# Optimization experiments

Hardware: AMD Instinct MI355X
Metric: run time of the kernel (lower is better)

## Reference

```python
import jax, jax.numpy as jnp
import numpy as np

TOPK = 13
ALPHA = 1.0
BETA = 6.0
REG_MAX = 16
W_MATCH, W_IOU, W_DFL, W_CONTRAST = 1.0, 7.5, 1.5, 1.0
EPS = 1e-7


def bbox_iou(a, b):
    # a, b: [..., 4] xyxy, broadcastable
    x1 = jnp.maximum(a[..., 0], b[..., 0])
    y1 = jnp.maximum(a[..., 1], b[..., 1])
    x2 = jnp.minimum(a[..., 2], b[..., 2])
    y2 = jnp.minimum(a[..., 3], b[..., 3])
    inter = jnp.clip(x2 - x1, 0.0) * jnp.clip(y2 - y1, 0.0)
    area_a = (a[..., 2] - a[..., 0]) * (a[..., 3] - a[..., 1])
    area_b = (b[..., 2] - b[..., 0]) * (b[..., 3] - b[..., 1])
    return inter / (area_a + area_b - inter + EPS)


def bbox_ciou(a, b):
    iou = bbox_iou(a, b)
    cw = jnp.maximum(a[..., 2], b[..., 2]) - jnp.minimum(a[..., 0], b[..., 0])
    ch = jnp.maximum(a[..., 3], b[..., 3]) - jnp.minimum(a[..., 1], b[..., 1])
    c2 = cw * cw + ch * ch + EPS
    rho2 = ((b[..., 0] + b[..., 2] - a[..., 0] - a[..., 2]) ** 2
            + (b[..., 1] + b[..., 3] - a[..., 1] - a[..., 3]) ** 2) * 0.25
    w1, h1 = a[..., 2] - a[..., 0], a[..., 3] - a[..., 1] + EPS
    w2, h2 = b[..., 2] - b[..., 0], b[..., 3] - b[..., 1] + EPS
    v = (4.0 / (np.pi ** 2)) * (jnp.arctan(w2 / h2) - jnp.arctan(w1 / h1)) ** 2
    alpha = jax.lax.stop_gradient(v / (v - iou + (1.0 + EPS)))
    return iou - rho2 / c2 - v * alpha


def _per_image(scores, boxes, logits, prompt, gts, anchors, stride, img_size):
    # scores [N], boxes [N,4], logits [N,4*REG_MAX], prompt [D], gts [G,4]
    N = scores.shape[0]
    dt = scores.dtype
    inside = ((anchors[None, :, 0] >= gts[:, None, 0]) & (anchors[None, :, 0] <= gts[:, None, 2])
              & (anchors[None, :, 1] >= gts[:, None, 1]) & (anchors[None, :, 1] <= gts[:, None, 3]))  # [G,N]
    ious = bbox_iou(boxes[None, :, :], gts[:, None, :])  # [G,N]
    prob = jax.nn.sigmoid(scores)
    align = jnp.where(inside, jnp.power(prob[None, :], ALPHA) * jnp.power(ious, BETA), -1.0)  # [G,N]
    top_vals, top_idx = jax.lax.top_k(align, TOPK)  # [G,TOPK]
    metric = jax.vmap(lambda i, v: jnp.full((N,), -2.0, dt).at[i].set(v))(top_idx, top_vals)  # [G,N]
    best = metric.max(axis=0)
    matched = metric.argmax(axis=0)  # [N]
    fg = best >= 0.0  # valid candidates always have align >= 0
    fgf = fg.astype(dt)
    overlap = jnp.take_along_axis(ious, matched[None, :], axis=0)[0]  # [N]
    target_scores = jnp.where(fg, jnp.maximum(overlap, 0.1), 0.0)
    target_boxes = jnp.where(fg[:, None], gts[matched], 0.0)  # [N,4]
    n_pos = fgf.sum()
    denom = jnp.maximum(n_pos, 1.0)
    # ---- BCE-with-logits (mean over all anchors) ----
    bce = jnp.maximum(scores, 0.0) - scores * target_scores + jnp.log1p(jnp.exp(-jnp.abs(scores)))
    match_loss = bce.mean()
    # ---- CIoU loss (masked mean over positives) ----
    ciou = bbox_ciou(boxes, target_boxes)
    iou_loss = jnp.sum((1.0 - ciou) * fgf) / denom
    # ---- DFL ----
    dist = jnp.concatenate([anchors - target_boxes[:, :2], target_boxes[:, 2:] - anchors], axis=-1) / stride
    dist = jnp.clip(dist, 0.0, REG_MAX - 1 - 0.01)  # [N,4]
    logsm = jax.nn.log_softmax(logits.reshape(N, 4, REG_MAX), axis=-1)
    tl = dist.astype(jnp.int32)
    tr = jnp.minimum(tl + 1, REG_MAX - 1)
    wl = tr.astype(dt) - dist
    wr = 1.0 - wl
    ll = -jnp.take_along_axis(logsm, tl[..., None], axis=-1)[..., 0]
    lr = -jnp.take_along_axis(logsm, tr[..., None], axis=-1)[..., 0]
    dfl = ll * wl + lr * wr  # [N,4]
    dfl_loss = jnp.sum(dfl * fgf[:, None]) / (4.0 * denom)
    # ---- Contrastive prompt alignment ----
    center = (target_boxes[:, :2] + target_boxes[:, 2:]) * 0.5 / jnp.maximum(img_size, 1.0)
    cv = center / jnp.maximum(jnp.linalg.norm(center, axis=-1, keepdims=True), 1e-12)
    pv = prompt[:2]
    pv = pv / jnp.maximum(jnp.linalg.norm(pv), 1e-12)
    contrast_loss = jnp.sum((1.0 - jnp.sum(cv * pv[None, :], axis=-1)) * fgf) / denom
    # ---- stats ----
    pos_score_sum = jnp.sum(prob * fgf)
    neg_score_sum = jnp.sum(prob * (1.0 - fgf))
    matched_iou_sum = jnp.sum(overlap * fgf)
    return match_loss, iou_loss, dfl_loss, contrast_loss, n_pos, pos_score_sum, neg_score_sum, matched_iou_sum


def setup_inputs() -> dict:
    img = 1280
    pts, strs = [], []
    for s in (8, 16, 32):
        n = img // s
        xs = (np.arange(n, dtype=np.float32) + 0.5) * s
        gx, gy = np.meshgrid(xs, xs)
        pts.append(np.stack([gx.ravel(), gy.ravel()], -1))
        strs.append(np.full((n * n, 1), s, np.float32))
    anchor_points = jnp.asarray(np.concatenate(pts).astype(np.float32))  # [33600,2]
    stride_tensor = jnp.asarray(np.concatenate(strs))  # [33600,1]
    N = anchor_points.shape[0]
    B, G = 16, 20
    k = jax.random.split(jax.random.key(0), 6)
    pred_scores = jax.random.normal(k[0], (B, N), jnp.float32) - 2.0
    off = jax.random.uniform(k[1], (B, N, 4), jnp.float32, 4.0, 80.0)
    ap = anchor_points[None, :, :]
    pred_boxes = jnp.concatenate([ap - off[..., :2], ap + off[..., 2:]], -1)
    box_distribution = jax.random.normal(k[2], (B, N, 4 * REG_MAX), jnp.float32)
    prompt_embedding = jax.random.normal(k[3], (B, 256), jnp.float32)
    c = jax.random.uniform(k[4], (B, G, 2), jnp.float32, 100.0, 1180.0)
    wh = jax.random.uniform(k[5], (B, G, 2), jnp.float32, 30.0, 300.0)
    gt_boxes = jnp.concatenate([c - wh * 0.5, c + wh * 0.5], -1)
    return {"pred_boxes": pred_boxes, "pred_scores": pred_scores, "anchor_points": anchor_points,
            "stride_tensor": stride_tensor, "box_distribution": box_distribution,
            "prompt_embedding": prompt_embedding, "gt_boxes": gt_boxes, "image_size": img}


def reference(pred_boxes, pred_scores, anchor_points, stride_tensor, box_distribution, prompt_embedding, gt_boxes, image_size):
    B, N = pred_scores.shape
    res = jax.vmap(_per_image, in_axes=(0, 0, 0, 0, 0, None, None, None))(
        pred_scores, pred_boxes, box_distribution, prompt_embedding, gt_boxes,
        anchor_points, stride_tensor, float(image_size))
    match, iou, dfl, contrast, n_pos, pos_sum, neg_sum, miou = [r.sum() for r in res]
    total_pos = n_pos
    total_neg = float(B * N) - total_pos
    nb = float(B)
    loss = (W_MATCH * match + W_IOU * iou + W_DFL * dfl + W_CONTRAST * contrast) / nb
    pd = jnp.maximum(total_pos, 1.0)
    nd = jnp.maximum(total_neg, 1.0)
    return (loss, match / nb, iou / nb, dfl / nb, contrast / nb,
            total_pos, total_neg, pos_sum / pd, neg_sum / nd, miou / pd)
```

## Files before the change

### kernel.cpp

```cpp
#include <hip/hip_runtime.h>
#include <math.h>

#define TOPK 13
#define REG_MAX 16
#define EPSF 1e-7f
#define MAXM 512
#define NEG_SENT -1e30f

__global__ __launch_bounds__(64) void topk_kernel(
    const float* __restrict__ boxes,
    const float* __restrict__ scores,
    const float* __restrict__ anchors,
    const float* __restrict__ gts,
    const int*   __restrict__ img_sz,
    float* __restrict__ topk_val,
    int*   __restrict__ topk_idx,
    int N, int G)
{
    const int bg   = blockIdx.x;
    const int b    = bg / G;
    const int lane = threadIdx.x;
    const int img  = img_sz[0];

    const float4 gt = ((const float4*)gts)[bg];

    float lv[TOPK];
    int   li[TOPK];
#pragma unroll
    for (int i = 0; i < TOPK; i++) { lv[i] = NEG_SENT; li[i] = 0; }

    const float4* bx = (const float4*)(boxes + (size_t)b * N * 4);
    const float*  sc = scores + (size_t)b * N;

    int base = 0;
#pragma unroll
    for (int L = 0; L < 3; L++) {
        const int s = 8 << L;
        const int n = img / s;
        const float fs = (float)s;
        int i0 = max(0,     (int)ceilf (gt.x / fs - 0.5f) - 1);
        int i1 = min(n - 1, (int)floorf(gt.z / fs - 0.5f) + 1);
        int j0 = max(0,     (int)ceilf (gt.y / fs - 0.5f) - 1);
        int j1 = min(n - 1, (int)floorf(gt.w / fs - 0.5f) + 1);
        if (i1 >= i0 && j1 >= j0) {
            const int W = i1 - i0 + 1;
            const int cnt = W * (j1 - j0 + 1);
            for (int t = lane; t < cnt; t += 64) {
                const int i = i0 + t % W;
                const int j = j0 + t / W;
                const int idx = base + j * n + i;
                const float ax = anchors[2*idx], ay = anchors[2*idx+1];
                if (ax < gt.x || ax > gt.z || ay < gt.y || ay > gt.w) continue;
                const float4 a = bx[idx];
                float x1 = fmaxf(a.x, gt.x), y1 = fmaxf(a.y, gt.y);
                float x2 = fminf(a.z, gt.z), y2 = fminf(a.w, gt.w);
                float inter  = fmaxf(x2 - x1, 0.0f) * fmaxf(y2 - y1, 0.0f);
                float area_a = (a.z - a.x) * (a.w - a.y);
                float area_b = (gt.z - gt.x) * (gt.w - gt.y);
                float iou  = inter / (area_a + area_b - inter + EPSF);
                float prob = 1.0f / (1.0f + expf(-sc[idx]));
                float i2 = iou * iou;
                float align = prob * i2 * i2 * i2;
                if (align > lv[TOPK-1]) {
                    float cv = align; int ci = idx;
#pragma unroll
                    for (int q = 0; q < TOPK; q++) {
                        if (cv > lv[q]) {
                            float tv = lv[q]; int ti = li[q];
                            lv[q] = cv; li[q] = ci; cv = tv; ci = ti;
                        }
                    }
                }
            }
        }
        base += n * n;
    }

    __shared__ float sval[64 * TOPK];
    __shared__ int   sidx[64 * TOPK];
#pragma unroll
    for (int i = 0; i < TOPK; i++) { sval[lane*TOPK+i] = lv[i]; sidx[lane*TOPK+i] = li[i]; }
    __builtin_amdgcn_s_waitcnt(0);

    int h = 0;
    for (int k = 0; k < TOPK; k++) {
        float v = (h < TOPK) ? sval[lane*TOPK + h] : NEG_SENT;
        float bv = v; int bs = lane;
#pragma unroll
        for (int off = 32; off > 0; off >>= 1) {
            float ov = __shfl_xor(bv, off);
            int   os = __shfl_xor(bs, off);
            if (ov > bv || (ov == bv && os < bs)) { bv = ov; bs = os; }
        }
        if (lane == bs) {
            topk_val[bg*TOPK + k] = sval[lane*TOPK + h];
            topk_idx[bg*TOPK + k] = sidx[lane*TOPK + h];
            h++;
        }
    }
}

__global__ __launch_bounds__(320) void fg_kernel(
    const float* __restrict__ boxes, const float* __restrict__ scores,
    const float* __restrict__ anchors, const float* __restrict__ strides,
    const float* __restrict__ logits, const float* __restrict__ prompt,
    const float* __restrict__ gts, const int* __restrict__ img_sz,
    const float* __restrict__ topk_val, const int* __restrict__ topk_idx,
    float* __restrict__ accs, int N, int G, int PD)
{
    const int b   = blockIdx.x;
    const int tid = threadIdx.x;
    const int M   = G * TOPK;

    __shared__ unsigned long long pk[MAXM];
    __shared__ int eis[MAXM];
    for (int e = tid; e < M; e += 320) {
        float v  = topk_val[b*M + e];
        int  idx = topk_idx[b*M + e];
        int  g   = e / TOPK;
        unsigned long long p = 0ull;
        if (v >= 0.0f) {
            p = (1ull << 62)
              | ((unsigned long long)(unsigned int)idx << 37)
              | ((unsigned long long)__float_as_uint(v) << 5)
              | (unsigned long long)(31 - g);
        }
        pk[e]  = p;
        eis[e] = idx;
    }
    __syncthreads();

    float imgf = fmaxf((float)img_sz[0], 1.0f);
    float p0 = prompt[(size_t)b*PD + 0], p1 = prompt[(size_t)b*PD + 1];
    float pn = fmaxf(sqrtf(p0*p0 + p1*p1), 1e-12f);
    p0 /= pn; p1 /= pn;

    float npos = 0.f, iou_sum = 0.f, dfl_sum = 0.f, con_sum = 0.f;
    float prob_sum = 0.f, corr_sum = 0.f, miou_sum = 0.f;

    for (int e = tid; e < M; e += 320) {
        const unsigned long long mine = pk[e];
        if (mine == 0ull) continue;
        bool lose = false;
        for (int e2 = 0; e2 < M; e2++) {
            unsigned long long p2 = pk[e2];
            lose |= (((p2 ^ mine) >> 37) == 0ull) & (p2 > mine);
        }
        if (lose) continue;

        const int idx = eis[e];
        const int g   = e / TOPK;

        const float4 a  = ((const float4*)(boxes + (size_t)b*N*4))[idx];
        const float4 tb = ((const float4*)gts)[b*G + g];
        float s    = scores[(size_t)b*N + idx];
        float prob = 1.0f / (1.0f + expf(-s));

        float x1 = fmaxf(a.x, tb.x), y1 = fmaxf(a.y, tb.y);
        float x2 = fminf(a.z, tb.z), y2 = fminf(a.w, tb.w);
        float inter  = fmaxf(x2 - x1, 0.f) * fmaxf(y2 - y1, 0.f);
        float area_a = (a.z - a.x) * (a.w - a.y);
        float area_b = (tb.z - tb.x) * (tb.w - tb.y);
        float iou = inter / (area_a + area_b - inter + EPSF);
        float tsc = fmaxf(iou, 0.1f);

        float cw = fmaxf(a.z, tb.z) - fminf(a.x, tb.x);
        float ch = fmaxf(a.w, tb.w) - fminf(a.y, tb.y);
        float c2 = cw*cw + ch*ch + EPSF;
        float dxc = tb.x + tb.z - a.x - a.z;
        float dyc = tb.y + tb.w - a.y - a.w;
        float rho2 = (dxc*dxc + dyc*dyc) * 0.25f;
        float w1 = a.z - a.x, h1 = a.w - a.y + EPSF;
        float w2 = tb.z - tb.x, h2 = tb.w - tb.y + EPSF;
        float dat = atanf(w2/h2) - atanf(w1/h1);
        float v   = 0.4052847345693511f * dat * dat;
        float alpha = v / (v - iou + (1.0f + EPSF));
        float ciou  = iou - rho2/c2 - v*alpha;
        iou_sum += 1.0f - ciou;

        float ax = anchors[2*idx], ay = anchors[2*idx+1];
        float st = strides[idx];
        float d4[4] = { (ax - tb.x)/st, (ay - tb.y)/st, (tb.z - ax)/st, (tb.w - ay)/st };
        const float4* lg4 = (const float4*)(logits + ((size_t)b*N + idx) * (4*REG_MAX));
        float dfl_n = 0.f;
#pragma unroll
        for (int sd = 0; sd < 4; sd++) {
            float4 q0 = lg4[sd*4+0], q1 = lg4[sd*4+1], q2 = lg4[sd*4+2], q3 = lg4[sd*4+3];
            float row[REG_MAX] = { q0.x,q0.y,q0.z,q0.w, q1.x,q1.y,q1.z,q1.w,
                                   q2.x,q2.y,q2.z,q2.w, q3.x,q3.y,q3.z,q3.w };
            float d = fminf(fmaxf(d4[sd], 0.0f), (float)(REG_MAX-1) - 0.01f);
            int tl = (int)d;
            int tr = min(tl + 1, REG_MAX - 1);
            float wl = (float)tr - d;
            float wr = 1.0f - wl;
            float m = row[0];
#pragma unroll
            for (int j = 1; j < REG_MAX; j++) m = fmaxf(m, row[j]);
            float se = 0.f;
#pragma unroll
            for (int j = 0; j < REG_MAX; j++) se += expf(row[j] - m);
            float lse = m + logf(se);
            dfl_n += (lse - row[tl]) * wl + (lse - row[tr]) * wr;
        }
        dfl_sum += dfl_n;

        float cx = (tb.x + tb.z) * 0.5f / imgf;
        float cy = (tb.y + tb.w) * 0.5f / imgf;
        float cn = fmaxf(sqrtf(cx*cx + cy*cy), 1e-12f);
        con_sum += 1.0f - (cx*p0 + cy*p1) / cn;

        npos     += 1.0f;
        prob_sum += prob;
        corr_sum += -s * tsc;
        miou_sum += iou;
    }

    float vals[7] = { npos, iou_sum, dfl_sum, con_sum, prob_sum, corr_sum, miou_sum };
#pragma unroll
    for (int k = 0; k < 7; k++) {
        float v = vals[k];
#pragma unroll
        for (int off = 32; off > 0; off >>= 1) v += __shfl_xor(v, off);
        vals[k] = v;
    }
    __shared__ float wred[5][7];
    const int w = tid >> 6, ln = tid & 63;
    if (ln == 0) {
#pragma unroll
        for (int k = 0; k < 7; k++) wred[w][k] = vals[k];
    }
    __syncthreads();
    if (tid == 0) {
        float fin[7];
#pragma unroll
        for (int k = 0; k < 7; k++) {
            float t = 0.f;
            for (int ww = 0; ww < 5; ww++) t += wred[ww][k];
            fin[k] = t;
        }
        float np    = fin[0];
        float denom = fmaxf(np, 1.0f);
        atomicAdd(&accs[0], fin[5]);
        atomicAdd(&accs[1], fin[1] / denom);
        atomicAdd(&accs[2], fin[2] / (4.0f*denom));
        atomicAdd(&accs[3], fin[3] / denom);
        atomicAdd(&accs[4], np);
        atomicAdd(&accs[5], fin[4]);
        atomicAdd(&accs[6], fin[6]);
    }
}

__global__ __launch_bounds__(256) void bce_kernel(
    const float* __restrict__ scores, float* __restrict__ accs, int total)
{
    const int tid = threadIdx.x;
    float bce0 = 0.f, prsum = 0.f;
    const int nvec = total >> 2;
    const float4* s4 = (const float4*)scores;
    for (int n = blockIdx.x*256 + tid; n < nvec; n += gridDim.x*256) {
        float4 v = s4[n];
        float ss[4] = { v.x, v.y, v.z, v.w };
#pragma unroll
        for (int q = 0; q < 4; q++) {
            float s = ss[q];
            bce0  += fmaxf(s, 0.0f) + log1pf(expf(-fabsf(s)));
            prsum += 1.0f / (1.0f + expf(-s));
        }
    }
    if (blockIdx.x == 0) {
        for (int n = (nvec << 2) + tid; n < total; n += 256) {
            float s = scores[n];
            bce0  += fmaxf(s, 0.0f) + log1pf(expf(-fabsf(s)));
            prsum += 1.0f / (1.0f + expf(-s));
        }
    }
    float v1 = bce0, v2 = prsum;
#pragma unroll
    for (int off = 32; off > 0; off >>= 1) {
        v1 += __shfl_xor(v1, off);
        v2 += __shfl_xor(v2, off);
    }
    __shared__ float r1[4], r2[4];
    const int w = tid >> 6, ln = tid & 63;
    if (ln == 0) { r1[w] = v1; r2[w] = v2; }
    __syncthreads();
    if (tid == 0) {
        atomicAdd(&accs[7], r1[0]+r1[1]+r1[2]+r1[3]);
        atomicAdd(&accs[8], r2[0]+r2[1]+r2[2]+r2[3]);
    }
}

__global__ void finalize_kernel(const float* __restrict__ accs,
                                float* __restrict__ out, int N, int B)
{
    if (threadIdx.x == 0 && blockIdx.x == 0) {
        float match = (accs[7] + accs[0]) / (float)N;
        float iou = accs[1], dfl = accs[2], con = accs[3];
        float tp  = accs[4];
        float tn  = (float)B * (float)N - tp;
        float nb  = (float)B;
        float loss = (1.0f*match + 7.5f*iou + 1.5f*dfl + 1.0f*con) / nb;
        float pd = fmaxf(tp, 1.0f), nd = fmaxf(tn, 1.0f);
        out[0] = loss;
        out[1] = match / nb;
        out[2] = iou / nb;
        out[3] = dfl / nb;
        out[4] = con / nb;
        out[5] = tp;
        out[6] = tn;
        out[7] = accs[5] / pd;
        out[8] = (accs[8] - accs[5]) / nd;
        out[9] = accs[6] / pd;
    }
}

extern "C" void kernel_launch(void* const* d_in, const int* in_sizes, int n_in,
                              void* d_out, int out_size, void* d_ws, size_t ws_size,
                              hipStream_t stream)
{
    const float* boxes   = (const float*)d_in[0];
    const float* scores  = (const float*)d_in[1];
    const float* anchors = (const float*)d_in[2];
    const float* strides = (const float*)d_in[3];
    const float* logits  = (const float*)d_in[4];
    const float* prompt  = (const float*)d_in[5];
    const float* gts     = (const float*)d_in[6];
    const int*   img     = (const int*)d_in[7];

    const int N  = in_sizes[2] / 2;
    const int B  = in_sizes[1] / N;
    const int G  = in_sizes[6] / (B * 4);
    const int PD = in_sizes[5] / B;

    float* out  = (float*)d_out;
    char*  ws   = (char*)d_ws;
    float* accs = (float*)ws;
    float* tkv  = (float*)(ws + 64);
    int*   tki  = (int*)(ws + 64 + (size_t)B*G*TOPK*sizeof(float));

    hipMemsetAsync(accs, 0, 64, stream);
    topk_kernel<<<B*G, 64, 0, stream>>>(boxes, scores, anchors, gts, img, tkv, tki, N, G);
    fg_kernel<<<B, 320, 0, stream>>>(boxes, scores, anchors, strides, logits, prompt,
                                     gts, img, tkv, tki, accs, N, G, PD);
    bce_kernel<<<512, 256, 0, stream>>>(scores, accs, B*N);
    finalize_kernel<<<1, 64, 0, stream>>>(accs, out, N, B);
}
```

Before: 280.7 us.

## Widen top-k blocks, split fg work per GT, replace atomics with partials

The top-k kernel now uses 256 threads per (image, GT) block with a two-level wave merge. It also computes anchor centres analytically from the grid index instead of loading the anchor array. The fg kernel is relaunched with one 64-thread block per (image, GT), each lane handling one top-k candidate, and per-block partials are written to a buffer. The finalize kernel now reduces those partials, which removes the per-image atomics. Computing anchors analytically assumes they follow the (i+0.5)*stride grid layout, and the finalize kernel assumes B <= 64.

```diff
diff --git a/kernel.cpp b/kernel.cpp
--- a/kernel.cpp
+++ b/kernel.cpp
@@ -7,10 +7,9 @@
 #define MAXM 512
 #define NEG_SENT -1e30f
 
-__global__ __launch_bounds__(64) void topk_kernel(
+__global__ __launch_bounds__(256) void topk_kernel(
     const float* __restrict__ boxes,
     const float* __restrict__ scores,
-    const float* __restrict__ anchors,
     const float* __restrict__ gts,
     const int*   __restrict__ img_sz,
     float* __restrict__ topk_val,
@@ -19,7 +18,9 @@
 {
     const int bg   = blockIdx.x;
     const int b    = bg / G;
-    const int lane = threadIdx.x;
+    const int tid  = threadIdx.x;
+    const int lane = tid & 63;
+    const int w    = tid >> 6;
     const int img  = img_sz[0];
 
     const float4 gt = ((const float4*)gts)[bg];
@@ -45,12 +46,13 @@
         if (i1 >= i0 && j1 >= j0) {
             const int W = i1 - i0 + 1;
             const int cnt = W * (j1 - j0 + 1);
-            for (int t = lane; t < cnt; t += 64) {
+            for (int t = tid; t < cnt; t += 256) {
                 const int i = i0 + t % W;
                 const int j = j0 + t / W;
+                const float ax = ((float)i + 0.5f) * fs;
+                const float ay = ((float)j + 0.5f) * fs;
+                if (ax < gt.x || ax > gt.z || ay < gt.y || ay > gt.w) continue;
                 const int idx = base + j * n + i;
-                const float ax = anchors[2*idx], ay = anchors[2*idx+1];
-                if (ax < gt.x || ax > gt.z || ay < gt.y || ay > gt.w) continue;
                 const float4 a = bx[idx];
                 float x1 = fmaxf(a.x, gt.x), y1 = fmaxf(a.y, gt.y);
                 float x2 = fminf(a.z, gt.z), y2 = fminf(a.w, gt.w);
@@ -76,15 +78,17 @@
         base += n * n;
     }
 
-    __shared__ float sval[64 * TOPK];
-    __shared__ int   sidx[64 * TOPK];
-#pragma unroll
-    for (int i = 0; i < TOPK; i++) { sval[lane*TOPK+i] = lv[i]; sidx[lane*TOPK+i] = li[i]; }
+    __shared__ float sval[256 * TOPK];
+    __shared__ int   sidx[256 * TOPK];
+#pragma unroll
+    for (int i = 0; i < TOPK; i++) { sval[tid*TOPK+i] = lv[i]; sidx[tid*TOPK+i] = li[i]; }
     __builtin_amdgcn_s_waitcnt(0);
 
+    __shared__ float wtv[4][TOPK];
+    __shared__ int   wti[4][TOPK];
     int h = 0;
     for (int k = 0; k < TOPK; k++) {
-        float v = (h < TOPK) ? sval[lane*TOPK + h] : NEG_SENT;
+        float v = (h < TOPK) ? sval[tid*TOPK + h] : NEG_SENT;
         float bv = v; int bs = lane;
 #pragma unroll
         for (int off = 32; off > 0; off >>= 1) {
@@ -93,126 +97,151 @@
             if (ov > bv || (ov == bv && os < bs)) { bv = ov; bs = os; }
         }
         if (lane == bs) {
-            topk_val[bg*TOPK + k] = sval[lane*TOPK + h];
-            topk_idx[bg*TOPK + k] = sidx[lane*TOPK + h];
+            wtv[w][k] = v;
+            wti[w][k] = sidx[tid*TOPK + h];
             h++;
         }
     }
-}
-
-__global__ __launch_bounds__(320) void fg_kernel(
+    __syncthreads();
+
+    if (w == 0) {
+        int hh = 0;
+        for (int k = 0; k < TOPK; k++) {
+            float v = (lane < 4) ? wtv[lane & 3][hh] : NEG_SENT;
+            float bv = v; int bs = lane;
+#pragma unroll
+            for (int off = 32; off > 0; off >>= 1) {
+                float ov = __shfl_xor(bv, off);
+                int   os = __shfl_xor(bs, off);
+                if (ov > bv || (ov == bv && os < bs)) { bv = ov; bs = os; }
+            }
+            if (lane == bs) {
+                topk_val[bg*TOPK + k] = v;
+                topk_idx[bg*TOPK + k] = wti[lane & 3][hh];
+                hh++;
+            }
+        }
+    }
+}
+
+__global__ __launch_bounds__(64) void fg_kernel(
     const float* __restrict__ boxes, const float* __restrict__ scores,
     const float* __restrict__ anchors, const float* __restrict__ strides,
     const float* __restrict__ logits, const float* __restrict__ prompt,
     const float* __restrict__ gts, const int* __restrict__ img_sz,
     const float* __restrict__ topk_val, const int* __restrict__ topk_idx,
-    float* __restrict__ accs, int N, int G, int PD)
-{
-    const int b   = blockIdx.x;
-    const int tid = threadIdx.x;
-    const int M   = G * TOPK;
+    float* __restrict__ part, int N, int G, int PD)
+{
+    const int bg   = blockIdx.x;
+    const int b    = bg / G;
+    const int g    = bg - b * G;
+    const int lane = threadIdx.x;
+    const int M    = G * TOPK;
 
     __shared__ unsigned long long pk[MAXM];
-    __shared__ int eis[MAXM];
-    for (int e = tid; e < M; e += 320) {
+    for (int e = lane; e < M; e += 64) {
         float v  = topk_val[b*M + e];
         int  idx = topk_idx[b*M + e];
-        int  g   = e / TOPK;
+        int  gg  = e / TOPK;
         unsigned long long p = 0ull;
         if (v >= 0.0f) {
             p = (1ull << 62)
               | ((unsigned long long)(unsigned int)idx << 37)
               | ((unsigned long long)__float_as_uint(v) << 5)
-              | (unsigned long long)(31 - g);
-        }
-        pk[e]  = p;
-        eis[e] = idx;
-    }
-    __syncthreads();
-
-    float imgf = fmaxf((float)img_sz[0], 1.0f);
-    float p0 = prompt[(size_t)b*PD + 0], p1 = prompt[(size_t)b*PD + 1];
-    float pn = fmaxf(sqrtf(p0*p0 + p1*p1), 1e-12f);
-    p0 /= pn; p1 /= pn;
+              | (unsigned long long)(31 - gg);
+        }
+        pk[e] = p;
+    }
+    __builtin_amdgcn_s_waitcnt(0);
 
     float npos = 0.f, iou_sum = 0.f, dfl_sum = 0.f, con_sum = 0.f;
     float prob_sum = 0.f, corr_sum = 0.f, miou_sum = 0.f;
 
-    for (int e = tid; e < M; e += 320) {
+    if (lane < TOPK) {
+        const int e = g*TOPK + lane;
         const unsigned long long mine = pk[e];
-        if (mine == 0ull) continue;
-        bool lose = false;
-        for (int e2 = 0; e2 < M; e2++) {
-            unsigned long long p2 = pk[e2];
-            lose |= (((p2 ^ mine) >> 37) == 0ull) & (p2 > mine);
-        }
-        if (lose) continue;
-
-        const int idx = eis[e];
-        const int g   = e / TOPK;
-
-        const float4 a  = ((const float4*)(boxes + (size_t)b*N*4))[idx];
-        const float4 tb = ((const float4*)gts)[b*G + g];
-        float s    = scores[(size_t)b*N + idx];
-        float prob = 1.0f / (1.0f + expf(-s));
-
-        float x1 = fmaxf(a.x, tb.x), y1 = fmaxf(a.y, tb.y);
-        float x2 = fminf(a.z, tb.z), y2 = fminf(a.w, tb.w);
-        float inter  = fmaxf(x2 - x1, 0.f) * fmaxf(y2 - y1, 0.f);
-        float area_a = (a.z - a.x) * (a.w - a.y);
-        float area_b = (tb.z - tb.x) * (tb.w - tb.y);
-        float iou = inter / (area_a + area_b - inter + EPSF);
-        float tsc = fmaxf(iou, 0.1f);
-
-        float cw = fmaxf(a.z, tb.z) - fminf(a.x, tb.x);
-        float ch = fmaxf(a.w, tb.w) - fminf(a.y, tb.y);
-        float c2 = cw*cw + ch*ch + EPSF;
-        float dxc = tb.x + tb.z - a.x - a.z;
-        float dyc = tb.y + tb.w - a.y - a.w;
-        float rho2 = (dxc*dxc + dyc*dyc) * 0.25f;
-        float w1 = a.z - a.x, h1 = a.w - a.y + EPSF;
-        float w2 = tb.z - tb.x, h2 = tb.w - tb.y + EPSF;
-        float dat = atanf(w2/h2) - atanf(w1/h1);
-        float v   = 0.4052847345693511f * dat * dat;
-        float alpha = v / (v - iou + (1.0f + EPSF));
-        float ciou  = iou - rho2/c2 - v*alpha;
-        iou_sum += 1.0f - ciou;
-
-        float ax = anchors[2*idx], ay = anchors[2*idx+1];
-        float st = strides[idx];
-        float d4[4] = { (ax - tb.x)/st, (ay - tb.y)/st, (tb.z - ax)/st, (tb.w - ay)/st };
-        const float4* lg4 = (const float4*)(logits + ((size_t)b*N + idx) * (4*REG_MAX));
-        float dfl_n = 0.f;
-#pragma unroll
-        for (int sd = 0; sd < 4; sd++) {
-            float4 q0 = lg4[sd*4+0], q1 = lg4[sd*4+1], q2 = lg4[sd*4+2], q3 = lg4[sd*4+3];
-            float row[REG_MAX] = { q0.x,q0.y,q0.z,q0.w, q1.x,q1.y,q1.z,q1.w,
-                                   q2.x,q2.y,q2.z,q2.w, q3.x,q3.y,q3.z,q3.w };
-            float d = fminf(fmaxf(d4[sd], 0.0f), (float)(REG_MAX-1) - 0.01f);
-            int tl = (int)d;
-            int tr = min(tl + 1, REG_MAX - 1);
-            float wl = (float)tr - d;
-            float wr = 1.0f - wl;
-            float m = row[0];
-#pragma unroll
-            for (int j = 1; j < REG_MAX; j++) m = fmaxf(m, row[j]);
-            float se = 0.f;
-#pragma unroll
-            for (int j = 0; j < REG_MAX; j++) se += expf(row[j] - m);
-            float lse = m + logf(se);
-            dfl_n += (lse - row[tl]) * wl + (lse - row[tr]) * wr;
-        }
-        dfl_sum += dfl_n;
-
-        float cx = (tb.x + tb.z) * 0.5f / imgf;
-        float cy = (tb.y + tb.w) * 0.5f / imgf;
-        float cn = fmaxf(sqrtf(cx*cx + cy*cy), 1e-12f);
-        con_sum += 1.0f - (cx*p0 + cy*p1) / cn;
-
-        npos     += 1.0f;
-        prob_sum += prob;
-        corr_sum += -s * tsc;
-        miou_sum += iou;
+        if (mine != 0ull) {
+            bool lose = false;
+            for (int e2 = 0; e2 < M; e2++) {
+                unsigned long long p2 = pk[e2];
+                lose |= (((p2 ^ mine) >> 37) == 0ull) & (p2 > mine);
+            }
+            if (!lose) {
+                const int idx = topk_idx[b*M + e];
+
+                const float4 a  = ((const float4*)(boxes + (size_t)b*N*4))[idx];
+                const float4 tb = ((const float4*)gts)[b*G + g];
+                float s    = scores[(size_t)b*N + idx];
+                float prob = 1.0f / (1.0f + expf(-s));
+
+                float x1 = fmaxf(a.x, tb.x), y1 = fmaxf(a.y, tb.y);
+                float x2 = fminf(a.z, tb.z), y2 = fminf(a.w, tb.w);
+                float inter  = fmaxf(x2 - x1, 0.f) * fmaxf(y2 - y1, 0.f);
+                float area_a = (a.z - a.x) * (a.w - a.y);
+                float area_b = (tb.z - tb.x) * (tb.w - tb.y);
+                float iou = inter / (area_a + area_b - inter + EPSF);
+                float tsc = fmaxf(iou, 0.1f);
+
+                float cw = fmaxf(a.z, tb.z) - fminf(a.x, tb.x);
+                float ch = fmaxf(a.w, tb.w) - fminf(a.y, tb.y);
+                float c2 = cw*cw + ch*ch + EPSF;
+                float dxc = tb.x + tb.z - a.x - a.z;
+                float dyc = tb.y + tb.w - a.y - a.w;
+                float rho2 = (dxc*dxc + dyc*dyc) * 0.25f;
+                float w1 = a.z - a.x, h1 = a.w - a.y + EPSF;
+                float w2 = tb.z - tb.x, h2 = tb.w - tb.y + EPSF;
+                float dat = atanf(w2/h2) - atanf(w1/h1);
+                float v   = 0.4052847345693511f * dat * dat;
+                float alpha = v / (v - iou + (1.0f + EPSF));
+                float ciou  = iou - rho2/c2 - v*alpha;
+                iou_sum = 1.0f - ciou;
+
+                float ax = anchors[2*idx], ay = anchors[2*idx+1];
+                float st = strides[idx];
+                float d4[4] = { (ax - tb.x)/st, (ay - tb.y)/st,
+                                (tb.z - ax)/st, (tb.w - ay)/st };
+                const float4* lg4 = (const float4*)(logits + ((size_t)b*N + idx) * (4*REG_MAX));
+                float dfl_n = 0.f;
+#pragma unroll
+                for (int sd = 0; sd < 4; sd++) {
+                    float4 q0 = lg4[sd*4+0], q1 = lg4[sd*4+1], q2 = lg4[sd*4+2], q3 = lg4[sd*4+3];
+                    float row[REG_MAX] = { q0.x,q0.y,q0.z,q0.w, q1.x,q1.y,q1.z,q1.w,
+                                           q2.x,q2.y,q2.z,q2.w, q3.x,q3.y,q3.z,q3.w };
+                    float d = fminf(fmaxf(d4[sd], 0.0f), (float)(REG_MAX-1) - 0.01f);
+                    int tl = (int)d;
+                    int tr = min(tl + 1, REG_MAX - 1);
+                    float wl = (float)tr - d;
+                    float wr = 1.0f - wl;
+                    float m = row[0];
+#pragma unroll
+                    for (int j = 1; j < REG_MAX; j++) m = fmaxf(m, row[j]);
+                    float se = 0.f;
+                    float rtl = row[0], rtr = row[0];
+#pragma unroll
+                    for (int j = 0; j < REG_MAX; j++) {
+                        se += expf(row[j] - m);
+                        rtl = (j == tl) ? row[j] : rtl;
+                        rtr = (j == tr) ? row[j] : rtr;
+                    }
+                    float lse = m + logf(se);
+                    dfl_n += (lse - rtl) * wl + (lse - rtr) * wr;
+                }
+                dfl_sum = dfl_n;
+
+                float imgf = fmaxf((float)img_sz[0], 1.0f);
+                float p0 = prompt[(size_t)b*PD + 0], p1 = prompt[(size_t)b*PD + 1];
+                float pn = fmaxf(sqrtf(p0*p0 + p1*p1), 1e-12f);
+                float cx = (tb.x + tb.z) * 0.5f / imgf;
+                float cy = (tb.y + tb.w) * 0.5f / imgf;
+                float cn = fmaxf(sqrtf(cx*cx + cy*cy), 1e-12f);
+                con_sum = 1.0f - (cx*(p0/pn) + cy*(p1/pn)) / cn;
+
+                npos     = 1.0f;
+                prob_sum = prob;
+                corr_sum = -s * tsc;
+                miou_sum = iou;
+            }
+        }
     }
 
     float vals[7] = { npos, iou_sum, dfl_sum, con_sum, prob_sum, corr_sum, miou_sum };
@@ -223,35 +252,15 @@
         for (int off = 32; off > 0; off >>= 1) v += __shfl_xor(v, off);
         vals[k] = v;
     }
-    __shared__ float wred[5][7];
-    const int w = tid >> 6, ln = tid & 63;
-    if (ln == 0) {
-#pragma unroll
-        for (int k = 0; k < 7; k++) wred[w][k] = vals[k];
-    }
-    __syncthreads();
-    if (tid == 0) {
-        float fin[7];
-#pragma unroll
-        for (int k = 0; k < 7; k++) {
-            float t = 0.f;
-            for (int ww = 0; ww < 5; ww++) t += wred[ww][k];
-            fin[k] = t;
-        }
-        float np    = fin[0];
-        float denom = fmaxf(np, 1.0f);
-        atomicAdd(&accs[0], fin[5]);
-        atomicAdd(&accs[1], fin[1] / denom);
-        atomicAdd(&accs[2], fin[2] / (4.0f*denom));
-        atomicAdd(&accs[3], fin[3] / denom);
-        atomicAdd(&accs[4], np);
-        atomicAdd(&accs[5], fin[4]);
-        atomicAdd(&accs[6], fin[6]);
+    if (lane == 0) {
+        float* p = part + (size_t)bg * 7;
+#pragma unroll
+        for (int k = 0; k < 7; k++) p[k] = vals[k];
     }
 }
 
 __global__ __launch_bounds__(256) void bce_kernel(
-    const float* __restrict__ scores, float* __restrict__ accs, int total)
+    const float* __restrict__ scores, float* __restrict__ glob, int total)
 {
     const int tid = threadIdx.x;
     float bce0 = 0.f, prsum = 0.f;
@@ -285,18 +294,47 @@
     if (ln == 0) { r1[w] = v1; r2[w] = v2; }
     __syncthreads();
     if (tid == 0) {
-        atomicAdd(&accs[7], r1[0]+r1[1]+r1[2]+r1[3]);
-        atomicAdd(&accs[8], r2[0]+r2[1]+r2[2]+r2[3]);
-    }
-}
-
-__global__ void finalize_kernel(const float* __restrict__ accs,
-                                float* __restrict__ out, int N, int B)
-{
-    if (threadIdx.x == 0 && blockIdx.x == 0) {
-        float match = (accs[7] + accs[0]) / (float)N;
-        float iou = accs[1], dfl = accs[2], con = accs[3];
-        float tp  = accs[4];
+        atomicAdd(&glob[0], r1[0]+r1[1]+r1[2]+r1[3]);
+        atomicAdd(&glob[1], r2[0]+r2[1]+r2[2]+r2[3]);
+    }
+}
+
+__global__ __launch_bounds__(64) void finalize_kernel(
+    const float* __restrict__ part, const float* __restrict__ glob,
+    float* __restrict__ out, int N, int B, int G)
+{
+    const int lane = threadIdx.x;
+    float np = 0.f, iouS = 0.f, dflS = 0.f, conS = 0.f;
+    float probS = 0.f, corrS = 0.f, miouS = 0.f;
+    if (lane < B) {
+        float a0=0,a1=0,a2=0,a3=0,a4=0,a5=0,a6=0;
+        const float* p = part + (size_t)lane * G * 7;
+        for (int g = 0; g < G; g++) {
+            a0 += p[g*7+0]; a1 += p[g*7+1]; a2 += p[g*7+2]; a3 += p[g*7+3];
+            a4 += p[g*7+4]; a5 += p[g*7+5]; a6 += p[g*7+6];
+        }
+        float denom = fmaxf(a0, 1.0f);
+        np    = a0;
+        iouS  = a1 / denom;
+        dflS  = a2 / (4.0f * denom);
+        conS  = a3 / denom;
+        probS = a4;
+        corrS = a5;
+        miouS = a6;
+    }
+    float vals[7] = { np, iouS, dflS, conS, probS, corrS, miouS };
+#pragma unroll
+    for (int k = 0; k < 7; k++) {
+        float v = vals[k];
+#pragma unroll
+        for (int off = 32; off > 0; off >>= 1) v += __shfl_xor(v, off);
+        vals[k] = v;
+    }
+    if (lane == 0) {
+        float bce0 = glob[0], prall = glob[1];
+        float match = (bce0 + vals[5]) / (float)N;
+        float iou = vals[1], dfl = vals[2], con = vals[3];
+        float tp  = vals[0];
         float tn  = (float)B * (float)N - tp;
         float nb  = (float)B;
         float loss = (1.0f*match + 7.5f*iou + 1.5f*dfl + 1.0f*con) / nb;
@@ -308,9 +346,9 @@
         out[4] = con / nb;
         out[5] = tp;
         out[6] = tn;
-        out[7] = accs[5] / pd;
-        out[8] = (accs[8] - accs[5]) / nd;
-        out[9] = accs[6] / pd;
+        out[7] = vals[4] / pd;
+        out[8] = (prall - vals[4]) / nd;
+        out[9] = vals[6] / pd;
     }
 }
 
@@ -334,14 +372,17 @@
 
     float* out  = (float*)d_out;
     char*  ws   = (char*)d_ws;
-    float* accs = (float*)ws;
-    float* tkv  = (float*)(ws + 64);
-    int*   tki  = (int*)(ws + 64 + (size_t)B*G*TOPK*sizeof(float));
-
-    hipMemsetAsync(accs, 0, 64, stream);
-    topk_kernel<<<B*G, 64, 0, stream>>>(boxes, scores, anchors, gts, img, tkv, tki, N, G);
-    fg_kernel<<<B, 320, 0, stream>>>(boxes, scores, anchors, strides, logits, prompt,
-                                     gts, img, tkv, tki, accs, N, G, PD);
-    bce_kernel<<<512, 256, 0, stream>>>(scores, accs, B*N);
-    finalize_kernel<<<1, 64, 0, stream>>>(accs, out, N, B);
-}
+    float* glob = (float*)ws;
+    float* part = (float*)(ws + 64);
+    size_t off  = 64 + (size_t)B * G * 7 * sizeof(float);
+    off = (off + 63) & ~(size_t)63;
+    float* tkv  = (float*)(ws + off);
+    int*   tki  = (int*)(ws + off + (size_t)B*G*TOPK*sizeof(float));
+
+    hipMemsetAsync(glob, 0, 64, stream);
+    topk_kernel<<<B*G, 256, 0, stream>>>(boxes, scores, gts, img, tkv, tki, N, G);
+    fg_kernel<<<B*G, 64, 0, stream>>>(boxes, scores, anchors, strides, logits, prompt,
+                                      gts, img, tkv, tki, part, N, G, PD);
+    bce_kernel<<<512, 256, 0, stream>>>(scores, glob, B*N);
+    finalize_kernel<<<1, 64, 0, stream>>>(part, glob, out, N, B, G);
+}
```

New measurement: 253.1 us. -9.8%, faster.
